# Kernel optimization log

Measured on AMD Instinct MI355X. Metric: run time of the kernel, lower is better.

The kernel has to match this reference:

```python
import jax, jax.numpy as jnp
import numpy as np

B, H, S, D = 4, 16, 2048, 64

def setup_inputs() -> dict:
    key = jax.random.key(0)
    kq, kk, kv = jax.random.split(key, 3)
    Q = jax.random.normal(kq, (B, H, S, D), dtype=jnp.float32)
    K = jax.random.normal(kk, (B, H, S, D), dtype=jnp.float32)
    V = jax.random.normal(kv, (B, H, S, D), dtype=jnp.float32)
    return {"Q": Q, "K": K, "V": V}

def reference(Q, K, V):
    d = Q.shape[-1]
    scale = jnp.sqrt(jnp.asarray(d, dtype=Q.dtype))
    # scores: [B, H, S, S]
    scores = jnp.einsum('bhqd,bhkd->bhqk', Q, K) / scale
    attn = jax.nn.softmax(scores, axis=-1)
    out = jnp.einsum('bhqk,bhkd->bhqd', attn, V)  # [B,H,S,D]
    # permute to [B,S,H,D] then merge heads -> [B,S,H*D]
    b, h, s, dd = out.shape
    return out.transpose(0, 2, 1, 3).reshape(b, s, h * dd)
```

## Files before the change

### kernel.cpp

```cpp
#include <hip/hip_runtime.h>
#include <hip/hip_bf16.h>


#define B_ 4
#define H_ 16
#define S_ 2048
#define D_ 64
#define BH 64
#define NKT 32
#define TILE_USH 4096
#define ARR_USH ((size_t)BH * NKT * TILE_USH)
#define WS_NEED (2 * ARR_USH * 2)
#define QSCALE 0.18033688011112042f

typedef float  f4 __attribute__((ext_vector_type(4)));
typedef short  s4 __attribute__((ext_vector_type(4)));
typedef short  s8 __attribute__((ext_vector_type(8)));
typedef unsigned short ushort_t;

__device__ __forceinline__ unsigned short f2bf(float x) {
  unsigned int u = __float_as_uint(x);
  u += 0x7fffu + ((u >> 16) & 1u);
  return (unsigned short)(u >> 16);
}
__device__ __forceinline__ unsigned int pk_bf16(float a, float b) {
  __hip_bfloat162 h = __float22bfloat162_rn(make_float2(a, b));
  union { __hip_bfloat162 h2; unsigned int u; } cv; cv.h2 = h; return cv.u;
}
__device__ __forceinline__ void splitbf_rne(float x, unsigned short& hi, unsigned short& lo) {
  hi = f2bf(x);
  float hf = __uint_as_float((unsigned int)hi << 16);
  lo = f2bf(x - hf);
}
__device__ __forceinline__ void splitbf(float x, unsigned short& hi, unsigned short& lo) {
  unsigned int u = __float_as_uint(x);
  hi = (unsigned short)(u >> 16);
  float hf = __uint_as_float(u & 0xffff0000u);
  lo = (unsigned short)(__float_as_uint(x - hf) >> 16);
}

typedef __attribute__((address_space(1))) const unsigned int* gas_t;
typedef __attribute__((address_space(3))) unsigned int* las_t;
__device__ __forceinline__ void gl_lds16(const void* g, void* l) {
  __builtin_amdgcn_global_load_lds((gas_t)g, (las_t)l, 16, 0, 0);
}

__global__ __launch_bounds__(256)
void prep(const float* __restrict__ K, const float* __restrict__ V,
          ushort_t* __restrict__ KH, ushort_t* __restrict__ VT) {
  __shared__ float Vf[64][68];
  const int tile = blockIdx.x;
  const int t = threadIdx.x;

  const float* vsrc = V + (size_t)tile * 4096;
  float4 vv[4];
  int srow[4], dcol[4];
  #pragma unroll
  for (int r = 0; r < 4; ++r) {
    int f = r * 256 + t; srow[r] = f >> 4; dcol[r] = (f & 15) << 2;
    vv[r] = *(const float4*)(vsrc + srow[r] * 64 + dcol[r]);
  }
  {
    const float* src0 = K + (size_t)tile * 4096;
    #pragma unroll
    for (int u = 0; u < 2; ++u) {
      unsigned int i = u * 256 + t;
      unsigned int row = i >> 3, c = (i & 7) ^ (row & 7);
      const float* src = src0 + row * 64 + c * 8;
      float4 a = *(const float4*)src;
      float4 b = *(const float4*)(src + 4);
      unsigned int d0 = pk_bf16(a.x, a.y), d1 = pk_bf16(a.z, a.w);
      unsigned int d2 = pk_bf16(b.x, b.y), d3 = pk_bf16(b.z, b.w);
      uint4 out = make_uint4(d0, d1, d2, d3);
      *(uint4*)(KH + (size_t)tile * TILE_USH + i * 8) = out;
    }
  }
  #pragma unroll
  for (int r = 0; r < 4; ++r) {
    int pcol = dcol[r] ^ (((srow[r] >> 3) & 3) << 2);
    *(float4*)&Vf[srow[r]][pcol] = vv[r];
  }
  __syncthreads();
  #pragma unroll
  for (int u = 0; u < 2; ++u) {
    unsigned int i = u * 256 + t;
    unsigned int drow = i >> 3, c = (i & 7) ^ (drow & 7);
    const unsigned int col = drow ^ ((c & 3) << 2);
    unsigned int d0 = pk_bf16(Vf[c * 8 + 0][col], Vf[c * 8 + 1][col]);
    unsigned int d1 = pk_bf16(Vf[c * 8 + 2][col], Vf[c * 8 + 3][col]);
    unsigned int d2 = pk_bf16(Vf[c * 8 + 4][col], Vf[c * 8 + 5][col]);
    unsigned int d3 = pk_bf16(Vf[c * 8 + 6][col], Vf[c * 8 + 7][col]);
    uint4 out = make_uint4(d0, d1, d2, d3);
    *(uint4*)(VT + (size_t)tile * TILE_USH + i * 8) = out;
  }
}

__global__ __launch_bounds__(256, 4)
void attn7(const float* __restrict__ Q, const ushort_t* __restrict__ KH,
           const ushort_t* __restrict__ VT, float* __restrict__ O) {
  __shared__ ushort_t KhS[2][TILE_USH];
  __shared__ ushort_t VtS[2][TILE_USH];
  __shared__ ushort_t Pb[4][1024];

  const int t    = threadIdx.x;
  const int w    = t >> 6;
  const int lane = t & 63;
  const int g    = lane >> 4;
  const int ln   = lane & 15;

  const unsigned int n = blockIdx.x;
  const int bh = (int)((n >> 7) * 8 + (n & 7));
  const int q0 = (int)(((n >> 3) & 15) * 128);

  const size_t tb = (size_t)bh * NKT * TILE_USH;
  const unsigned int cb = w * 128;

  #pragma unroll
  for (int j = 0; j < 2; ++j) {
    const unsigned int ch = cb + 64u * j;
    const size_t go = tb + (size_t)(ch + lane) * 8;
    gl_lds16(KH + go, &KhS[0][ch * 8]);
    gl_lds16(VT + go, &VtS[0][ch * 8]);
  }

  s8 qfh[2][2], qfl[2][2];
  #pragma unroll
  for (int sub = 0; sub < 2; ++sub) {
    const int q = q0 + 32 * w + 16 * sub + ln;
    #pragma unroll
    for (int ks = 0; ks < 2; ++ks) {
      const float* qp = Q + ((size_t)bh * S_ + q) * 64 + 32 * ks + 8 * g;
      float4 a = *(const float4*)qp;
      float4 b = *(const float4*)(qp + 4);
      float xs[8] = {a.x, a.y, a.z, a.w, b.x, b.y, b.z, b.w};
      s8 hv, lv;
      #pragma unroll
      for (int j = 0; j < 8; ++j) {
        unsigned short h, lo; splitbf_rne(xs[j] * QSCALE, h, lo);
        hv[j] = (short)h; lv[j] = (short)lo;
      }
      qfh[sub][ks] = hv; qfl[sub][ks] = lv;
    }
  }

  f4 oacc[2][4];
  f4 lacc[2];
  #pragma unroll
  for (int s = 0; s < 2; ++s) {
    lacc[s] = (f4)0.0f;
    #pragma unroll
    for (int d = 0; d < 4; ++d) oacc[s][d] = (f4)0.0f;
  }

  s8 ones;
  #pragma unroll
  for (int j = 0; j < 8; ++j) ones[j] = (short)0x3F80;

  unsigned int foff[2];
  #pragma unroll
  for (int ks = 0; ks < 2; ++ks)
    foff[ks] = (unsigned)ln * 128u + (unsigned)(((4 * ks + g) ^ (ln & 7)) * 16);

  const unsigned int pro = (unsigned)ln * 64u + (unsigned)((g ^ (ln >> 2)) & 3) * 16u;

  for (int kt = 0; kt < NKT; ++kt) {
    const int cur = kt & 1;
    __syncthreads();

    if (kt + 1 < NKT) {
      const size_t tbase = tb + (size_t)(kt + 1) * TILE_USH;
      const int nb = cur ^ 1;
      #pragma unroll
      for (int j = 0; j < 2; ++j) {
        const unsigned int ch = cb + 64u * j;
        const size_t go = tbase + (size_t)(ch + lane) * 8;
        gl_lds16(KH + go, &KhS[nb][ch * 8]);
        gl_lds16(VT + go, &VtS[nb][ch * 8]);
      }
    }

    const char* khb = (const char*)&KhS[cur][0];
    const char* vtb = (const char*)&VtS[cur][0];

    #pragma unroll
    for (int h = 0; h < 2; ++h) {
      #pragma unroll
      for (int ntl = 0; ntl < 2; ++ntl) {
        const int nt = 2 * h + ntl;
        s8 kh0 = *(const s8*)(khb + nt * 2048 + foff[0]);
        s8 kh1 = *(const s8*)(khb + nt * 2048 + foff[1]);
        const unsigned int c1 = (16u * (unsigned)ntl + (unsigned)ln) ^ (8u * (unsigned)g);
        #pragma unroll
        for (int sub = 0; sub < 2; ++sub) {
          f4 sc = (f4)0.0f;
          sc = __builtin_amdgcn_mfma_f32_16x16x32_bf16(qfh[sub][0], kh0, sc, 0, 0, 0);
          sc = __builtin_amdgcn_mfma_f32_16x16x32_bf16(qfl[sub][0], kh0, sc, 0, 0, 0);
          sc = __builtin_amdgcn_mfma_f32_16x16x32_bf16(qfh[sub][1], kh1, sc, 0, 0, 0);
          sc = __builtin_amdgcn_mfma_f32_16x16x32_bf16(qfl[sub][1], kh1, sc, 0, 0, 0);
          float p0 = __builtin_amdgcn_exp2f(sc[0]);
          float p1 = __builtin_amdgcn_exp2f(sc[1]);
          float p2 = __builtin_amdgcn_exp2f(sc[2]);
          float p3 = __builtin_amdgcn_exp2f(sc[3]);
          unsigned int pk01 = pk_bf16(p0, p1);
          unsigned int pk23 = pk_bf16(p2, p3);
          ushort_t* base = &Pb[w][sub * 512];
          base[(4 * g + 0) * 32 + c1] = (ushort_t)pk01;
          base[(4 * g + 1) * 32 + c1] = (ushort_t)(pk01 >> 16);
          base[(4 * g + 2) * 32 + c1] = (ushort_t)pk23;
          base[(4 * g + 3) * 32 + c1] = (ushort_t)(pk23 >> 16);
        }
      }

      s8 pa[2];
      #pragma unroll
      for (int sub = 0; sub < 2; ++sub) {
        pa[sub] = *(const s8*)((const char*)&Pb[w][0] + sub * 1024 + pro);
        lacc[sub] = __builtin_amdgcn_mfma_f32_16x16x32_bf16(pa[sub], ones, lacc[sub], 0, 0, 0);
      }
      #pragma unroll
      for (int dt = 0; dt < 4; ++dt) {
        s8 vb = *(const s8*)(vtb + dt * 2048 + foff[h]);
        #pragma unroll
        for (int sub = 0; sub < 2; ++sub)
          oacc[sub][dt] = __builtin_amdgcn_mfma_f32_16x16x32_bf16(pa[sub], vb, oacc[sub][dt], 0, 0, 0);
      }
    }
  }

  const int b = bh >> 4, hh = bh & 15;
  #pragma unroll
  for (int sub = 0; sub < 2; ++sub)
    #pragma unroll
    for (int r = 0; r < 4; ++r) {
      const float inv = 1.0f / lacc[sub][r];
      const int q = q0 + 32 * w + 16 * sub + 4 * g + r;
      float* dst = O + ((size_t)b * S_ + q) * (H_ * D_) + hh * 64;
      #pragma unroll
      for (int dt = 0; dt < 4; ++dt)
        dst[16 * dt + ln] = oacc[sub][dt][r] * inv;
    }
}

#define KQ_STR 72
#define VP_STR 76
__global__ __launch_bounds__(256, 2)
void attn_mfma(const float* __restrict__ Q, const float* __restrict__ K,
               const float* __restrict__ V, float* __restrict__ O) {
  __shared__ __align__(16) unsigned short Qh[64][KQ_STR];
  __shared__ __align__(16) unsigned short Ql[64][KQ_STR];
  __shared__ __align__(16) unsigned short Kh[64][KQ_STR];
  __shared__ __align__(16) unsigned short Kl[64][KQ_STR];
  __shared__ __align__(16) unsigned short Vt[64][VP_STR];
  __shared__ __align__(16) unsigned short Pb2[4][16][VP_STR];
  const int t = threadIdx.x, w = t >> 6, lane = t & 63, g = lane >> 4, ln = lane & 15;
  const int bh = blockIdx.x, q0 = blockIdx.y * 64;
  const size_t base = (size_t)bh * S_ * D_;
  {
    const float* Qg = Q + base + (size_t)q0 * D_;
    #pragma unroll
    for (int r = 0; r < 4; ++r) {
      int f = r * 256 + t, row = f >> 4, c4 = (f & 15) << 2;
      float4 v = *(const float4*)(Qg + row * 64 + c4);
      s4 hv, lv; unsigned short hb, lb;
      splitbf(v.x * 0.125f, hb, lb); hv[0] = (short)hb; lv[0] = (short)lb;
      splitbf(v.y * 0.125f, hb, lb); hv[1] = (short)hb; lv[1] = (short)lb;
      splitbf(v.z * 0.125f, hb, lb); hv[2] = (short)hb; lv[2] = (short)lb;
      splitbf(v.w * 0.125f, hb, lb); hv[3] = (short)hb; lv[3] = (short)lb;
      *(s4*)&Qh[row][c4] = hv; *(s4*)&Ql[row][c4] = lv;
    }
  }
  __syncthreads();
  s8 qfh[2], qfl[2];
  #pragma unroll
  for (int ks = 0; ks < 2; ++ks) {
    qfh[ks] = *(const s8*)&Qh[16 * w + ln][ks * 32 + 8 * g];
    qfl[ks] = *(const s8*)&Ql[16 * w + ln][ks * 32 + 8 * g];
  }
  f4 oacc[4]; float m[4], l[4];
  #pragma unroll
  for (int i = 0; i < 4; ++i) { oacc[i] = (f4)0.0f; m[i] = -1e30f; l[i] = 0.0f; }
  const float* Kg = K + base; const float* Vg = V + base;
  float4 kreg[4], vreg[4];
  #pragma unroll
  for (int r = 0; r < 4; ++r) {
    int f = r * 256 + t, row = f >> 4, c4 = (f & 15) << 2;
    kreg[r] = *(const float4*)(Kg + row * 64 + c4);
  }
  #pragma unroll
  for (int j = 0; j < 2; ++j) {
    int it = j * 256 + t, kp = it >> 4, c4 = (it & 15) << 2;
    vreg[2 * j] = *(const float4*)(Vg + (2 * kp) * 64 + c4);
    vreg[2 * j + 1] = *(const float4*)(Vg + (2 * kp + 1) * 64 + c4);
  }
  for (int kt = 0; kt < S_ / 64; ++kt) {
    __syncthreads();
    #pragma unroll
    for (int r = 0; r < 4; ++r) {
      int f = r * 256 + t, row = f >> 4, c4 = (f & 15) << 2;
      float4 v = kreg[r];
      s4 hv, lv; unsigned short hb, lb;
      splitbf(v.x, hb, lb); hv[0] = (short)hb; lv[0] = (short)lb;
      splitbf(v.y, hb, lb); hv[1] = (short)hb; lv[1] = (short)lb;
      splitbf(v.z, hb, lb); hv[2] = (short)hb; lv[2] = (short)lb;
      splitbf(v.w, hb, lb); hv[3] = (short)hb; lv[3] = (short)lb;
      *(s4*)&Kh[row][c4] = hv; *(s4*)&Kl[row][c4] = lv;
    }
    #pragma unroll
    for (int j = 0; j < 2; ++j) {
      int it = j * 256 + t, kp = it >> 4, c4 = (it & 15) << 2;
      float4 a = vreg[2 * j], b = vreg[2 * j + 1];
      float xa[4] = {a.x, a.y, a.z, a.w}, xb[4] = {b.x, b.y, b.z, b.w};
      #pragma unroll
      for (int i = 0; i < 4; ++i) {
        unsigned int pk = (unsigned int)f2bf(xa[i]) | ((unsigned int)f2bf(xb[i]) << 16);
        *(unsigned int*)&Vt[c4 + i][2 * kp] = pk;
      }
    }
    if (kt + 1 < S_ / 64) {
      const float* Kt = Kg + (size_t)(kt + 1) * 4096;
      const float* Vn = Vg + (size_t)(kt + 1) * 4096;
      #pragma unroll
      for (int r = 0; r < 4; ++r) {
        int f = r * 256 + t, row = f >> 4, c4 = (f & 15) << 2;
        kreg[r] = *(const float4*)(Kt + row * 64 + c4);
      }
      #pragma unroll
      for (int j = 0; j < 2; ++j) {
        int it = j * 256 + t, kp = it >> 4, c4 = (it & 15) << 2;
        vreg[2 * j] = *(const float4*)(Vn + (2 * kp) * 64 + c4);
        vreg[2 * j + 1] = *(const float4*)(Vn + (2 * kp + 1) * 64 + c4);
      }
    }
    __syncthreads();
    f4 sacc[4];
    #pragma unroll
    for (int nt = 0; nt < 4; ++nt) sacc[nt] = (f4)0.0f;
    #pragma unroll
    for (int nt = 0; nt < 4; ++nt)
      #pragma unroll
      for (int ks = 0; ks < 2; ++ks) {
        s8 kh = *(const s8*)&Kh[16 * nt + ln][ks * 32 + 8 * g];
        s8 kl = *(const s8*)&Kl[16 * nt + ln][ks * 32 + 8 * g];
        sacc[nt] = __builtin_amdgcn_mfma_f32_16x16x32_bf16(qfh[ks], kh, sacc[nt], 0, 0, 0);
        sacc[nt] = __builtin_amdgcn_mfma_f32_16x16x32_bf16(qfl[ks], kh, sacc[nt], 0, 0, 0);
        sacc[nt] = __builtin_amdgcn_mfma_f32_16x16x32_bf16(qfh[ks], kl, sacc[nt], 0, 0, 0);
      }
    #pragma unroll
    for (int r = 0; r < 4; ++r) {
      float rm = fmaxf(fmaxf(sacc[0][r], sacc[1][r]), fmaxf(sacc[2][r], sacc[3][r]));
      rm = fmaxf(rm, __shfl_xor(rm, 1)); rm = fmaxf(rm, __shfl_xor(rm, 2));
      rm = fmaxf(rm, __shfl_xor(rm, 4)); rm = fmaxf(rm, __shfl_xor(rm, 8));
      float mn = fmaxf(m[r], rm);
      float alpha = __expf(m[r] - mn); m[r] = mn;
      float p0 = __expf(sacc[0][r] - mn), p1 = __expf(sacc[1][r] - mn);
      float p2 = __expf(sacc[2][r] - mn), p3 = __expf(sacc[3][r] - mn);
      float rs = p0 + p1 + p2 + p3;
      rs += __shfl_xor(rs, 1); rs += __shfl_xor(rs, 2);
      rs += __shfl_xor(rs, 4); rs += __shfl_xor(rs, 8);
      l[r] = l[r] * alpha + rs;
      oacc[0][r] *= alpha; oacc[1][r] *= alpha; oacc[2][r] *= alpha; oacc[3][r] *= alpha;
      const int row = 4 * g + r;
      Pb2[w][row][ln] = f2bf(p0); Pb2[w][row][ln + 16] = f2bf(p1);
      Pb2[w][row][ln + 32] = f2bf(p2); Pb2[w][row][ln + 48] = f2bf(p3);
    }
    #pragma unroll
    for (int ks = 0; ks < 2; ++ks) {
      s4 pa0 = *(const s4*)&Pb2[w][ln][ks * 32 + 8 * g];
      s4 pa1 = *(const s4*)&Pb2[w][ln][ks * 32 + 8 * g + 4];
      s8 pa = __builtin_shufflevector(pa0, pa1, 0, 1, 2, 3, 4, 5, 6, 7);
      #pragma unroll
      for (int dt = 0; dt < 4; ++dt) {
        s4 vb0 = *(const s4*)&Vt[16 * dt + ln][ks * 32 + 8 * g];
        s4 vb1 = *(const s4*)&Vt[16 * dt + ln][ks * 32 + 8 * g + 4];
        s8 vb = __builtin_shufflevector(vb0, vb1, 0, 1, 2, 3, 4, 5, 6, 7);
        oacc[dt] = __builtin_amdgcn_mfma_f32_16x16x32_bf16(pa, vb, oacc[dt], 0, 0, 0);
      }
    }
  }
  const int b = bh >> 4, h = bh & 15;
  #pragma unroll
  for (int r = 0; r < 4; ++r) {
    const int q = q0 + 16 * w + 4 * g + r;
    const float inv = 1.0f / l[r];
    float* dst = O + ((size_t)b * S_ + q) * (H_ * D_) + h * 64;
    #pragma unroll
    for (int dt = 0; dt < 4; ++dt) dst[16 * dt + ln] = oacc[dt][r] * inv;
  }
}

extern "C" void kernel_launch(void* const* d_in, const int* in_sizes, int n_in,
                              void* d_out, int out_size, void* d_ws, size_t ws_size,
                              hipStream_t stream) {
  const float* Q = (const float*)d_in[0];
  const float* K = (const float*)d_in[1];
  const float* V = (const float*)d_in[2];
  float* Out = (float*)d_out;
  if (ws_size >= WS_NEED) {
    ushort_t* KHp = (ushort_t*)d_ws;
    ushort_t* VTp = KHp + ARR_USH;
    hipLaunchKernelGGL(prep, dim3(2048), dim3(256), 0, stream, K, V, KHp, VTp);
    hipLaunchKernelGGL(attn7, dim3(1024), dim3(256), 0, stream, Q, KHp, VTp, Out);
  } else {
    hipLaunchKernelGGL(attn_mfma, dim3(BH, S_ / 64), dim3(256), 0, stream, Q, K, V, Out);
  }
}
```

Baseline: 221.5 us.

## Keep softmax probabilities in registers via transposed QK MFMA and lane shuffles

Computes scores as K·Qᵀ by swapping the MFMA operands, so each lane holds probabilities in the orientation needed for the P·V A-operand. The missing pieces are rearranged with two rounds of cross-lane shuffles, and the per-wave LDS staging buffer with its scattered 16-bit stores and reloads is removed. Launch bounds rise from 4 to 5 blocks per CU to use the freed LDS and registers. The risk is extra shuffle and select instructions, and possible register pressure at the higher occupancy target.

```diff
diff --git a/kernel.cpp b/kernel.cpp
--- a/kernel.cpp
+++ b/kernel.cpp
@@ -95,12 +95,11 @@
   }
 }
 
-__global__ __launch_bounds__(256, 4)
-void attn7(const float* __restrict__ Q, const ushort_t* __restrict__ KH,
+__global__ __launch_bounds__(256, 5)
+void attn8(const float* __restrict__ Q, const ushort_t* __restrict__ KH,
            const ushort_t* __restrict__ VT, float* __restrict__ O) {
   __shared__ ushort_t KhS[2][TILE_USH];
   __shared__ ushort_t VtS[2][TILE_USH];
-  __shared__ ushort_t Pb[4][1024];
 
   const int t    = threadIdx.x;
   const int w    = t >> 6;
@@ -161,7 +160,8 @@
   for (int ks = 0; ks < 2; ++ks)
     foff[ks] = (unsigned)ln * 128u + (unsigned)(((4 * ks + g) ^ (ln & 7)) * 16);
 
-  const unsigned int pro = (unsigned)ln * 64u + (unsigned)((g ^ (ln >> 2)) & 3) * 16u;
+  const bool glt2 = (g < 2);
+  const bool sr   = (g == 0) || (g == 3);
 
   for (int kt = 0; kt < NKT; ++kt) {
     const int cur = kt & 1;
@@ -184,39 +184,49 @@
 
     #pragma unroll
     for (int h = 0; h < 2; ++h) {
-      #pragma unroll
-      for (int ntl = 0; ntl < 2; ++ntl) {
-        const int nt = 2 * h + ntl;
-        s8 kh0 = *(const s8*)(khb + nt * 2048 + foff[0]);
-        s8 kh1 = *(const s8*)(khb + nt * 2048 + foff[1]);
-        const unsigned int c1 = (16u * (unsigned)ntl + (unsigned)ln) ^ (8u * (unsigned)g);
-        #pragma unroll
-        for (int sub = 0; sub < 2; ++sub) {
-          f4 sc = (f4)0.0f;
-          sc = __builtin_amdgcn_mfma_f32_16x16x32_bf16(qfh[sub][0], kh0, sc, 0, 0, 0);
-          sc = __builtin_amdgcn_mfma_f32_16x16x32_bf16(qfl[sub][0], kh0, sc, 0, 0, 0);
-          sc = __builtin_amdgcn_mfma_f32_16x16x32_bf16(qfh[sub][1], kh1, sc, 0, 0, 0);
-          sc = __builtin_amdgcn_mfma_f32_16x16x32_bf16(qfl[sub][1], kh1, sc, 0, 0, 0);
-          float p0 = __builtin_amdgcn_exp2f(sc[0]);
-          float p1 = __builtin_amdgcn_exp2f(sc[1]);
-          float p2 = __builtin_amdgcn_exp2f(sc[2]);
-          float p3 = __builtin_amdgcn_exp2f(sc[3]);
-          unsigned int pk01 = pk_bf16(p0, p1);
-          unsigned int pk23 = pk_bf16(p2, p3);
-          ushort_t* base = &Pb[w][sub * 512];
-          base[(4 * g + 0) * 32 + c1] = (ushort_t)pk01;
-          base[(4 * g + 1) * 32 + c1] = (ushort_t)(pk01 >> 16);
-          base[(4 * g + 2) * 32 + c1] = (ushort_t)pk23;
-          base[(4 * g + 3) * 32 + c1] = (ushort_t)(pk23 >> 16);
-        }
-      }
+      s8 k00 = *(const s8*)(khb + (2 * h + 0) * 2048 + foff[0]);
+      s8 k01 = *(const s8*)(khb + (2 * h + 0) * 2048 + foff[1]);
+      s8 k10 = *(const s8*)(khb + (2 * h + 1) * 2048 + foff[0]);
+      s8 k11 = *(const s8*)(khb + (2 * h + 1) * 2048 + foff[1]);
 
       s8 pa[2];
       #pragma unroll
       for (int sub = 0; sub < 2; ++sub) {
-        pa[sub] = *(const s8*)((const char*)&Pb[w][0] + sub * 1024 + pro);
+        f4 s0 = (f4)0.0f, s1 = (f4)0.0f;
+        s0 = __builtin_amdgcn_mfma_f32_16x16x32_bf16(k00, qfh[sub][0], s0, 0, 0, 0);
+        s0 = __builtin_amdgcn_mfma_f32_16x16x32_bf16(k00, qfl[sub][0], s0, 0, 0, 0);
+        s0 = __builtin_amdgcn_mfma_f32_16x16x32_bf16(k01, qfh[sub][1], s0, 0, 0, 0);
+        s0 = __builtin_amdgcn_mfma_f32_16x16x32_bf16(k01, qfl[sub][1], s0, 0, 0, 0);
+        s1 = __builtin_amdgcn_mfma_f32_16x16x32_bf16(k10, qfh[sub][0], s1, 0, 0, 0);
+        s1 = __builtin_amdgcn_mfma_f32_16x16x32_bf16(k10, qfl[sub][0], s1, 0, 0, 0);
+        s1 = __builtin_amdgcn_mfma_f32_16x16x32_bf16(k11, qfh[sub][1], s1, 0, 0, 0);
+        s1 = __builtin_amdgcn_mfma_f32_16x16x32_bf16(k11, qfl[sub][1], s1, 0, 0, 0);
+
+        unsigned int a0 = pk_bf16(__builtin_amdgcn_exp2f(s0[0]),
+                                  __builtin_amdgcn_exp2f(s0[1]));
+        unsigned int a1 = pk_bf16(__builtin_amdgcn_exp2f(s0[2]),
+                                  __builtin_amdgcn_exp2f(s0[3]));
+        unsigned int b0 = pk_bf16(__builtin_amdgcn_exp2f(s1[0]),
+                                  __builtin_amdgcn_exp2f(s1[1]));
+        unsigned int b1 = pk_bf16(__builtin_amdgcn_exp2f(s1[2]),
+                                  __builtin_amdgcn_exp2f(s1[3]));
+
+        unsigned int t0 = glt2 ? b0 : a0, t1 = glt2 ? b1 : a1;
+        unsigned int r0 = (unsigned int)__shfl_xor((int)t0, 32);
+        unsigned int r1 = (unsigned int)__shfl_xor((int)t1, 32);
+        unsigned int own0 = (g == 1) ? a0 : b0, own1 = (g == 1) ? a1 : b1;
+        unsigned int u0 = sr ? r0 : own0, u1 = sr ? r1 : own1;
+        unsigned int q0v = (unsigned int)__shfl_xor((int)u0, 16);
+        unsigned int q1v = (unsigned int)__shfl_xor((int)u1, 16);
+        union { unsigned int u[4]; s8 v; } cvp;
+        cvp.u[0] = (g == 0) ? a0 : (g == 2) ? r0 : q0v;
+        cvp.u[1] = (g == 0) ? a1 : (g == 2) ? r1 : q1v;
+        cvp.u[2] = (g == 3) ? b0 : (g == 1) ? r0 : q0v;
+        cvp.u[3] = (g == 3) ? b1 : (g == 1) ? r1 : q1v;
+        pa[sub] = cvp.v;
         lacc[sub] = __builtin_amdgcn_mfma_f32_16x16x32_bf16(pa[sub], ones, lacc[sub], 0, 0, 0);
       }
+
       #pragma unroll
       for (int dt = 0; dt < 4; ++dt) {
         s8 vb = *(const s8*)(vtb + dt * 2048 + foff[h]);
@@ -399,7 +409,7 @@
     ushort_t* KHp = (ushort_t*)d_ws;
     ushort_t* VTp = KHp + ARR_USH;
     hipLaunchKernelGGL(prep, dim3(2048), dim3(256), 0, stream, K, V, KHp, VTp);
-    hipLaunchKernelGGL(attn7, dim3(1024), dim3(256), 0, stream, Q, KHp, VTp, Out);
+    hipLaunchKernelGGL(attn8, dim3(1024), dim3(256), 0, stream, Q, KHp, VTp, Out);
   } else {
     hipLaunchKernelGGL(attn_mfma, dim3(BH, S_ / 64), dim3(256), 0, stream, Q, K, V, Out);
   }
```

Result: slower. 620.5 us (+180.1%).
